# Kernel optimization log

Measured on AMD Instinct MI355X. Metric: run time of the kernel, lower is better.

The kernel has to match this reference:

```python
import jax, jax.numpy as jnp
import numpy as np

T, B, D, H = 512, 64, 512, 512

def setup_inputs() -> dict:
    key = jax.random.key(0)
    ks = jax.random.split(key, 14)
    s = 0.02
    inp = {
        "inputs": jax.random.normal(ks[0], (T, B, D), dtype=jnp.float32),
        # gate linears: weight [D+H, H] (transposed torch layout), bias [H]
        "Wf": jax.random.normal(ks[1], (D + H, H), dtype=jnp.float32) * s,
        "bf": jax.random.normal(ks[2], (H,), dtype=jnp.float32) * s,
        "Wi": jax.random.normal(ks[3], (D + H, H), dtype=jnp.float32) * s,
        "bi": jax.random.normal(ks[4], (H,), dtype=jnp.float32) * s,
        "Wg": jax.random.normal(ks[5], (D + H, H), dtype=jnp.float32) * s,
        "bg": jax.random.normal(ks[6], (H,), dtype=jnp.float32) * s,
        "Wo": jax.random.normal(ks[7], (D + H, H), dtype=jnp.float32) * s,
        "bo": jax.random.normal(ks[8], (H,), dtype=jnp.float32) * s,
        # residual linears on hidden state: [H, H], no bias
        "Rf": jax.random.normal(ks[9], (H, H), dtype=jnp.float32) * s,
        "Ri": jax.random.normal(ks[10], (H, H), dtype=jnp.float32) * s,
        "Rg": jax.random.normal(ks[11], (H, H), dtype=jnp.float32) * s,
        "Ro": jax.random.normal(ks[12], (H, H), dtype=jnp.float32) * s,
    }
    return inp


def reference(inputs, Wf, bf, Wi, bi, Wg, bg, Wo, bo, Rf, Ri, Rg, Ro):
    # QLSTM forward (eval mode, gate_dropout inactive). states=None -> zeros.
    batch = inputs.shape[1]
    hidden = Wf.shape[1]
    h0 = jnp.zeros((batch, hidden), dtype=inputs.dtype)
    c0 = jnp.zeros((batch, hidden), dtype=inputs.dtype)

    # Fuse the 4 gate GEMMs into one [D+H, 4H] matmul and the 4 residual
    # GEMMs into one [H, 4H] matmul (same math, fewer launches).
    W4 = jnp.concatenate([Wf, Wi, Wg, Wo], axis=1)   # [D+H, 4H]
    b4 = jnp.concatenate([bf, bi, bg, bo], axis=0)   # [4H]
    R4 = jnp.concatenate([Rf, Ri, Rg, Ro], axis=1)   # [H, 4H]

    def step(carry, x):
        hx, cx = carry
        combined = jnp.concatenate([x, hx], axis=1)            # [B, D+H]
        z = combined @ W4 + b4 + hx @ R4                        # [B, 4H]
        f, i, g, o = jnp.split(z, 4, axis=1)
        f = jax.nn.sigmoid(f)
        i = jax.nn.sigmoid(i)
        g = jnp.tanh(g)
        o = jax.nn.sigmoid(o)
        cx = f * cx + i * g
        hx = o * jnp.tanh(cx)
        return (hx, cx), hx

    (hx, cx), stacked = jax.lax.scan(step, (h0, c0), inputs)
    return stacked, hx, cx
```

## Files before the change

kernel.cpp:

```cpp
#include <hip/hip_runtime.h>
#include <hip/hip_bf16.h>

typedef __attribute__((ext_vector_type(8))) short s16x8;
typedef __attribute__((ext_vector_type(4))) float f32x4;

__device__ __forceinline__ ushort f2bf(float x) {
  __hip_bfloat16 b = __float2bfloat16(x);
  return *reinterpret_cast<ushort*>(&b);
}

__device__ __forceinline__ float sigm_fast(float z) {
  return __builtin_amdgcn_rcpf(1.0f + __builtin_amdgcn_exp2f(z * -1.44269504088896f));
}

__global__ __launch_bounds__(256) void pack_weights(
    const float* __restrict__ Wf, const float* __restrict__ Wi,
    const float* __restrict__ Wg, const float* __restrict__ Wo,
    const float* __restrict__ Rf, const float* __restrict__ Ri,
    const float* __restrict__ Rg, const float* __restrict__ Ro,
    const float* __restrict__ bfp, const float* __restrict__ bip,
    const float* __restrict__ bgp, const float* __restrict__ bop,
    ushort* __restrict__ Wx, ushort* __restrict__ Rs, float* __restrict__ bp)
{
  const int p = blockIdx.x * 8 + (threadIdx.x >> 5);
  const int kk = (threadIdx.x & 31) * 16;
  const int gate = p & 3;
  const int hcol = (p >> 5) * 8 + ((p >> 4) & 1) * 4 + ((p & 15) >> 2);
  const float* W = (gate == 0) ? Wf : (gate == 1) ? Wi : (gate == 2) ? Wg : Wo;
  const float* R = (gate == 0) ? Rf : (gate == 1) ? Ri : (gate == 2) ? Rg : Ro;
  union { ushort u[16]; s16x8 v[2]; } wb, rb;
#pragma unroll
  for (int e = 0; e < 16; ++e) {
    const int k = kk + e;
    wb.u[e] = f2bf(W[(size_t)k * 512 + hcol]);
    rb.u[e] = f2bf(W[(size_t)(512 + k) * 512 + hcol] + R[(size_t)k * 512 + hcol]);
  }
  *(s16x8*)(Wx + (size_t)p * 512 + kk)     = wb.v[0];
  *(s16x8*)(Wx + (size_t)p * 512 + kk + 8) = wb.v[1];
  *(s16x8*)(Rs + (size_t)p * 512 + kk)     = rb.v[0];
  *(s16x8*)(Rs + (size_t)p * 512 + kk + 8) = rb.v[1];
  if ((threadIdx.x & 31) == 0) {
    const float* B = (gate == 0) ? bfp : (gate == 1) ? bip : (gate == 2) ? bgp : bop;
    bp[p] = B[hcol];
  }
}

__global__ __launch_bounds__(256) void swizzle_x(
    const float* __restrict__ x, ushort* __restrict__ xsw)
{
  __shared__ ushort xl[64 * 520];
  const int t = blockIdx.x;
  const int tid = threadIdx.x;
  const float4* x4 = (const float4*)(x + (size_t)t * 32768);
#pragma unroll 4
  for (int j = 0; j < 32; ++j) {
    const int i4 = j * 256 + tid;
    const float4 v = x4[i4];
    const int base = i4 * 4;
    const int row = base >> 9;
    const int col = base & 511;
    ushort4 u;
    u.x = f2bf(v.x); u.y = f2bf(v.y); u.z = f2bf(v.z); u.w = f2bf(v.w);
    *(ushort4*)(&xl[row * 520 + col]) = u;
  }
  __syncthreads();
#pragma unroll 4
  for (int j = 0; j < 16; ++j) {
    const int F = j * 256 + tid;
    const int l = F & 63;
    const int kc = (F >> 6) & 15;
    const int mt = F >> 10;
    const int row = mt * 16 + (l & 15);
    const int k0 = kc * 32 + (l >> 4) * 8;
    const s16x8 v = *(const s16x8*)(&xl[row * 520 + k0]);
    *(s16x8*)(&xsw[((size_t)t * 4096 + F) * 8]) = v;
  }
}

__global__ __launch_bounds__(512, 1) void zx_gemm(
    const ushort* __restrict__ xsw, const ushort* __restrict__ Wx,
    float* __restrict__ zx, int t0, int tcnt)
{
  __shared__ ushort lbuf[32768];
  const int pg = blockIdx.x;
  const int tgrp = blockIdx.y;
  const int tid = threadIdx.x;
  const int wid = tid >> 6;
  const int lane = tid & 63;
  const int mpair = wid >> 2;
  const int np = wid & 3;
  const int q = pg * 4 + np;
  const int l15 = lane & 15;
  const int hi = lane >> 4;

  s16x8 Bg[2][16];
#pragma unroll
  for (int nt = 0; nt < 2; ++nt)
#pragma unroll
    for (int kc = 0; kc < 16; ++kc)
      Bg[nt][kc] = *(const s16x8*)(Wx + (size_t)(q * 32 + nt * 16 + l15) * 512 + kc * 32 + hi * 8);

  for (int tt = 0; tt < tcnt; ++tt) {
    const int tl = tgrp * tcnt + tt;
    const int t = t0 + tl;
#pragma unroll
    for (int j = 0; j < 8; ++j) {
      const int fid = j * 512 + tid;
      *(s16x8*)(&lbuf[(size_t)fid * 8]) =
          *(const s16x8*)(xsw + ((size_t)t * 4096 + fid) * 8);
    }
    __syncthreads();
#pragma unroll
    for (int a = 0; a < 2; ++a) {
      const int mt = mpair * 2 + a;
      f32x4 acc0 = {0.f, 0.f, 0.f, 0.f};
      f32x4 acc1 = {0.f, 0.f, 0.f, 0.f};
#pragma unroll
      for (int kc = 0; kc < 16; ++kc) {
        const s16x8 af = *(const s16x8*)(&lbuf[((size_t)(mt * 16 + kc) * 64 + lane) * 8]);
        acc0 = __builtin_amdgcn_mfma_f32_16x16x32_bf16(af, Bg[0][kc], acc0, 0, 0, 0);
        acc1 = __builtin_amdgcn_mfma_f32_16x16x32_bf16(af, Bg[1][kc], acc1, 0, 0, 0);
      }
      float* o = zx + ((((size_t)tl * 4 + mt) * 64 + q) * 64 + lane) * 8;
      *(f32x4*)(o)     = acc0;
      *(f32x4*)(o + 4) = acc1;
    }
    __syncthreads();
  }
}

__global__ __launch_bounds__(512, 1) void rec_kernel(
    const ushort* __restrict__ Rs, const float* __restrict__ bp,
    const float* __restrict__ zx, ushort* __restrict__ hbuf,
    float* __restrict__ csave, int* __restrict__ cnt,
    float* __restrict__ dout, int t0, int CH)
{
  __shared__ ushort hsl[8192];
  const int bid = blockIdx.x;
  const int g = bid & 3;
  const int tid = threadIdx.x;
  const int wid = tid >> 6;
  const int lane = tid & 63;
  const int q = (bid >> 2) * 8 + wid;
  const int gate = lane & 3;
  const int l15 = lane & 15;
  const int hi = lane >> 4;

  s16x8 Brg[2][16];
#pragma unroll
  for (int nt = 0; nt < 2; ++nt)
#pragma unroll
    for (int kc = 0; kc < 16; ++kc)
      Brg[nt][kc] = *(const s16x8*)(Rs + (size_t)(q * 32 + nt * 16 + l15) * 512 + kc * 32 + hi * 8);

  const float b0 = bp[q * 32 + l15];
  const float b1 = bp[q * 32 + 16 + l15];

  float cst[2][4];
  float* csp = csave + ((size_t)(bid * 8 + wid) * 64 + lane) * 8;
  if (t0 == 0) {
#pragma unroll
    for (int i = 0; i < 2; ++i)
#pragma unroll
      for (int r = 0; r < 4; ++r) cst[i][r] = 0.0f;
  } else {
#pragma unroll
    for (int i = 0; i < 2; ++i)
#pragma unroll
      for (int r = 0; r < 4; ++r) cst[i][r] = csp[i * 4 + r];
  }

  const int srow = hi * 4 + gate;
  const int hcol0 = q * 8 + (l15 >> 2);

  const int crow = tid >> 5;
  const int cbyte = (tid & 31) * 32;
  const int cswz = (crow & 7) << 4;
  const int abase = l15 * 1024 + hi * 16;
  const int aswz = (l15 & 7) << 4;

  int* const cptr = cnt + g * 64;

  const float* zp = zx + ((((size_t)0 * 4 + g) * 64 + q) * 64 + lane) * 8;
  float4 z0 = *(const float4*)zp;
  float4 z1 = *(const float4*)(zp + 4);

  for (int tl = 0; tl < CH; ++tl) {
    const int t = t0 + tl;

    if (tl > 0) {
      const int target = t * 8;
      while (__hip_atomic_load(cptr, __ATOMIC_RELAXED, __HIP_MEMORY_SCOPE_AGENT) < target) {}
      asm volatile("" ::: "memory");
    }

    {
      const ushort* hsrc = hbuf + ((size_t)tl * 4 + g) * 8192;
      const s16x8 v0 = *(const s16x8*)(hsrc + crow * 512 + (cbyte >> 1));
      const s16x8 v1 = *(const s16x8*)(hsrc + crow * 512 + (cbyte >> 1) + 8);
      *(s16x8*)(&hsl[(crow * 1024 + (cbyte ^ cswz)) >> 1]) = v0;
      *(s16x8*)(&hsl[(crow * 1024 + ((cbyte + 16) ^ cswz)) >> 1]) = v1;
    }
    __syncthreads();

    f32x4 acc0 = {0.f, 0.f, 0.f, 0.f};
    f32x4 acc1 = {0.f, 0.f, 0.f, 0.f};
#pragma unroll
    for (int kc = 0; kc < 16; ++kc) {
      const s16x8 a = *(const s16x8*)(&hsl[((abase + kc * 64) ^ aswz) >> 1]);
      acc0 = __builtin_amdgcn_mfma_f32_16x16x32_bf16(a, Brg[0][kc], acc0, 0, 0, 0);
      acc1 = __builtin_amdgcn_mfma_f32_16x16x32_bf16(a, Brg[1][kc], acc1, 0, 0, 0);
    }

    float h_out[2][4];
#pragma unroll
    for (int nt = 0; nt < 2; ++nt) {
#pragma unroll
      for (int r = 0; r < 4; ++r) {
        float z = (nt ? acc1[r] : acc0[r]);
        z += nt ? ((r == 0) ? z1.x : (r == 1) ? z1.y : (r == 2) ? z1.z : z1.w)
                : ((r == 0) ? z0.x : (r == 1) ? z0.y : (r == 2) ? z0.z : z0.w);
        z += nt ? b1 : b0;
        const float zz = (gate == 2) ? z + z : z;
        const float s = sigm_fast(zz);
        const float act = (gate == 2) ? (s + s - 1.0f) : s;
        const int ai = __float_as_int(act);
        const float fv = __int_as_float(__builtin_amdgcn_mov_dpp(ai, 0x00, 0xF, 0xF, true));
        const float iv = __int_as_float(__builtin_amdgcn_mov_dpp(ai, 0x55, 0xF, 0xF, true));
        const float gv = __int_as_float(__builtin_amdgcn_mov_dpp(ai, 0xAA, 0xF, 0xF, true));
        const float ov = __int_as_float(__builtin_amdgcn_mov_dpp(ai, 0xFF, 0xF, 0xF, true));
        const float cn = fmaf(fv, cst[nt][r], iv * gv);
        cst[nt][r] = cn;
        const float s2 = sigm_fast(cn + cn);
        h_out[nt][r] = ov * (s2 + s2 - 1.0f);
      }
    }

    float hv[2], cv[2];
#pragma unroll
    for (int nt = 0; nt < 2; ++nt) {
      hv[nt] = (gate == 0) ? h_out[nt][0] : (gate == 1) ? h_out[nt][1]
             : (gate == 2) ? h_out[nt][2] : h_out[nt][3];
      cv[nt] = (gate == 0) ? cst[nt][0] : (gate == 1) ? cst[nt][1]
             : (gate == 2) ? cst[nt][2] : cst[nt][3];
    }

    {
      ushort* hn = hbuf + ((size_t)(tl + 1) * 4 + g) * 8192;
#pragma unroll
      for (int nt = 0; nt < 2; ++nt)
        __hip_atomic_store(&hn[srow * 512 + hcol0 + nt * 4], f2bf(hv[nt]),
                           __ATOMIC_RELAXED, __HIP_MEMORY_SCOPE_AGENT);
      if (tl == CH - 1) {
        ushort* h0 = hbuf + (size_t)g * 8192;
#pragma unroll
        for (int nt = 0; nt < 2; ++nt)
          h0[srow * 512 + hcol0 + nt * 4] = f2bf(hv[nt]);
      }
    }
    asm volatile("s_waitcnt vmcnt(0)" ::: "memory");
    __syncthreads();
    if (tid == 0)
      __hip_atomic_fetch_add(cptr, 1, __ATOMIC_RELAXED, __HIP_MEMORY_SCOPE_AGENT);

    if (tl + 1 < CH) {
      const float* zn = zx + ((((size_t)(tl + 1) * 4 + g) * 64 + q) * 64 + lane) * 8;
      z0 = *(const float4*)zn;
      z1 = *(const float4*)(zn + 4);
    }
    {
      const size_t drow = (size_t)(g * 16 + srow) * 512;
#pragma unroll
      for (int nt = 0; nt < 2; ++nt)
        dout[(size_t)t * 32768 + drow + hcol0 + nt * 4] = hv[nt];
      if (t == 511) {
#pragma unroll
        for (int nt = 0; nt < 2; ++nt) {
          dout[(size_t)16777216 + drow + hcol0 + nt * 4] = hv[nt];
          dout[(size_t)16809984 + drow + hcol0 + nt * 4] = cv[nt];
        }
      }
    }
  }

#pragma unroll
  for (int i = 0; i < 2; ++i)
#pragma unroll
    for (int r = 0; r < 4; ++r) csp[i * 4 + r] = cst[i][r];
}

extern "C" void kernel_launch(void* const* d_in, const int* in_sizes, int n_in,
                              void* d_out, int out_size, void* d_ws, size_t ws_size,
                              hipStream_t stream)
{
  const float* x   = (const float*)d_in[0];
  const float* Wf  = (const float*)d_in[1];
  const float* bfp = (const float*)d_in[2];
  const float* Wi  = (const float*)d_in[3];
  const float* bip = (const float*)d_in[4];
  const float* Wg  = (const float*)d_in[5];
  const float* bgp = (const float*)d_in[6];
  const float* Wo  = (const float*)d_in[7];
  const float* bop = (const float*)d_in[8];
  const float* Rf  = (const float*)d_in[9];
  const float* Ri  = (const float*)d_in[10];
  const float* Rg  = (const float*)d_in[11];
  const float* Ro  = (const float*)d_in[12];
  float* dout = (float*)d_out;
  char* ws = (char*)d_ws;

  const size_t o_Wx  = 0;
  const size_t o_Rs  = o_Wx + 2097152;
  const size_t o_bp  = o_Rs + 2097152;
  const size_t o_xsw = o_bp + 8192;
  const size_t o_zx  = o_xsw + 33554432;

  int CH = 64;
  while (CH > 4) {
    const size_t need = o_zx + (size_t)CH * 524288 + (size_t)(CH + 1) * 65536
                      + 524288 + 1024;
    if (need <= ws_size) break;
    CH >>= 1;
  }
  const size_t o_hb = o_zx + (size_t)CH * 524288;
  const size_t o_cs = o_hb + (size_t)(CH + 1) * 65536;
  const size_t o_fl = o_cs + 524288;

  ushort* Wx  = (ushort*)(ws + o_Wx);
  ushort* Rs  = (ushort*)(ws + o_Rs);
  float*  bp  = (float*)(ws + o_bp);
  ushort* xsw = (ushort*)(ws + o_xsw);
  float*  zx  = (float*)(ws + o_zx);
  ushort* hb  = (ushort*)(ws + o_hb);
  float*  csv = (float*)(ws + o_cs);
  int*    fl  = (int*)(ws + o_fl);

  pack_weights<<<256, 256, 0, stream>>>(Wf, Wi, Wg, Wo, Rf, Ri, Rg, Ro,
                                        bfp, bip, bgp, bop, Wx, Rs, bp);
  swizzle_x<<<512, 256, 0, stream>>>(x, xsw);
  hipMemsetAsync(hb, 0, 65536, stream);
  hipMemsetAsync(fl, 0, 1024, stream);

  const int nch = 512 / CH;
  for (int c = 0; c < nch; ++c) {
    const int G = (CH < 16) ? CH : 16;
    zx_gemm<<<dim3(16, G), 512, 0, stream>>>(xsw, Wx, zx, c * CH, CH / G);
    rec_kernel<<<32, 512, 0, stream>>>(Rs, bp, zx, hb, csv, fl, dout, c * CH, CH);
  }
}
```

Measured before the change: 1.787 ms.

## Process two batch groups per block with interleaved recurrent steps on half the blocks

The recurrent kernel now launches 16 blocks instead of 32. Each block handles two batch groups (A and B) and interleaves their recurrent GEMM, gate math and publish phases, so the wait on one group's flag overlaps with compute for the other. Hidden-state publishing is staged through shared memory and written as 64-bit atomic stores from 16 lanes instead of scattered 16-bit stores, and the counter stride changes. The risk is that per-step serial work per block doubles, which can lengthen the critical path. The layout of the saved c-state also changes.

New measurement: 3.144 ms. 76.0% more time.

```diff
diff --git a/kernel.cpp b/kernel.cpp
--- a/kernel.cpp
+++ b/kernel.cpp
@@ -135,39 +135,47 @@
     float* __restrict__ csave, int* __restrict__ cnt,
     float* __restrict__ dout, int t0, int CH)
 {
-  __shared__ ushort hsl[8192];
+  __shared__ ushort hslA[8192];
+  __shared__ ushort hslB[8192];
+  __shared__ ushort tbuf[1024];
+
   const int bid = blockIdx.x;
-  const int g = bid & 3;
+  const int team = bid >> 3;
   const int tid = threadIdx.x;
   const int wid = tid >> 6;
   const int lane = tid & 63;
-  const int q = (bid >> 2) * 8 + wid;
+  const int q = (bid & 7) * 8 + wid;
+  const int gA = team * 2;
+  const int gB = team * 2 + 1;
   const int gate = lane & 3;
   const int l15 = lane & 15;
   const int hi = lane >> 4;
 
-  s16x8 Brg[2][16];
+  f32x4 Brg[2][16];
 #pragma unroll
   for (int nt = 0; nt < 2; ++nt)
 #pragma unroll
-    for (int kc = 0; kc < 16; ++kc)
-      Brg[nt][kc] = *(const s16x8*)(Rs + (size_t)(q * 32 + nt * 16 + l15) * 512 + kc * 32 + hi * 8);
+    for (int kc = 0; kc < 16; ++kc) {
+      Brg[nt][kc] = *(const f32x4*)(Rs + (size_t)(q * 32 + nt * 16 + l15) * 512 + kc * 32 + hi * 8);
+      asm volatile("" : "+v"(Brg[nt][kc]));
+    }
 
   const float b0 = bp[q * 32 + l15];
   const float b1 = bp[q * 32 + 16 + l15];
 
-  float cst[2][4];
-  float* csp = csave + ((size_t)(bid * 8 + wid) * 64 + lane) * 8;
+  float cA[2][4], cB[2][4];
+  float* cspA = csave + ((size_t)((bid * 8 + wid) * 64 + lane) * 2 + 0) * 8;
+  float* cspB = cspA + 8;
   if (t0 == 0) {
 #pragma unroll
     for (int i = 0; i < 2; ++i)
 #pragma unroll
-      for (int r = 0; r < 4; ++r) cst[i][r] = 0.0f;
+      for (int r = 0; r < 4; ++r) { cA[i][r] = 0.0f; cB[i][r] = 0.0f; }
   } else {
 #pragma unroll
     for (int i = 0; i < 2; ++i)
 #pragma unroll
-      for (int r = 0; r < 4; ++r) cst[i][r] = csp[i * 4 + r];
+      for (int r = 0; r < 4; ++r) { cA[i][r] = cspA[i * 4 + r]; cB[i][r] = cspB[i * 4 + r]; }
   }
 
   const int srow = hi * 4 + gate;
@@ -176,117 +184,174 @@
   const int crow = tid >> 5;
   const int cbyte = (tid & 31) * 32;
   const int cswz = (crow & 7) << 4;
+  const int srcofs = crow * 512 + (cbyte >> 1);
+  const int wofs0 = (crow * 1024 + (cbyte ^ cswz)) >> 1;
+  const int wofs1 = (crow * 1024 + ((cbyte + 16) ^ cswz)) >> 1;
   const int abase = l15 * 1024 + hi * 16;
   const int aswz = (l15 & 7) << 4;
 
-  int* const cptr = cnt + g * 64;
-
-  const float* zp = zx + ((((size_t)0 * 4 + g) * 64 + q) * 64 + lane) * 8;
-  float4 z0 = *(const float4*)zp;
-  float4 z1 = *(const float4*)(zp + 4);
+  int* const cptrA = cnt + gA * 16;
+  int* const cptrB = cnt + gB * 16;
+
+  const float* zpA = zx + (((size_t)0 * 4 + gA) * 64 + q) * 64 * 8 + (size_t)lane * 8;
+  const float* zpB = zx + (((size_t)0 * 4 + gB) * 64 + q) * 64 * 8 + (size_t)lane * 8;
+  float4 zA0 = *(const float4*)zpA, zA1 = *(const float4*)(zpA + 4);
+  float4 zB0 = *(const float4*)zpB, zB1 = *(const float4*)(zpB + 4);
+
+#define GATES(ACC0, ACC1, Z0, Z1, CST, HV0, HV1, CV0, CV1)                      \
+  {                                                                              \
+    float h_[2][4];                                                              \
+    _Pragma("unroll")                                                            \
+    for (int nt = 0; nt < 2; ++nt) {                                             \
+      _Pragma("unroll")                                                          \
+      for (int r = 0; r < 4; ++r) {                                              \
+        float z = (nt ? (ACC1)[r] : (ACC0)[r]);                                  \
+        z += nt ? ((r==0)?(Z1).x:(r==1)?(Z1).y:(r==2)?(Z1).z:(Z1).w)             \
+                : ((r==0)?(Z0).x:(r==1)?(Z0).y:(r==2)?(Z0).z:(Z0).w);            \
+        z += nt ? b1 : b0;                                                       \
+        const float zz = (gate == 2) ? z + z : z;                                \
+        const float s = sigm_fast(zz);                                           \
+        const float act = (gate == 2) ? (s + s - 1.0f) : s;                      \
+        const int ai = __float_as_int(act);                                      \
+        const float fv = __int_as_float(__builtin_amdgcn_mov_dpp(ai, 0x00, 0xF, 0xF, true)); \
+        const float iv = __int_as_float(__builtin_amdgcn_mov_dpp(ai, 0x55, 0xF, 0xF, true)); \
+        const float gv = __int_as_float(__builtin_amdgcn_mov_dpp(ai, 0xAA, 0xF, 0xF, true)); \
+        const float ov = __int_as_float(__builtin_amdgcn_mov_dpp(ai, 0xFF, 0xF, 0xF, true)); \
+        const float cn = fmaf(fv, CST[nt][r], iv * gv);                          \
+        CST[nt][r] = cn;                                                         \
+        const float s2 = sigm_fast(cn + cn);                                     \
+        h_[nt][r] = ov * (s2 + s2 - 1.0f);                                       \
+      }                                                                          \
+    }                                                                            \
+    HV0 = (gate==0)?h_[0][0]:(gate==1)?h_[0][1]:(gate==2)?h_[0][2]:h_[0][3];     \
+    HV1 = (gate==0)?h_[1][0]:(gate==1)?h_[1][1]:(gate==2)?h_[1][2]:h_[1][3];     \
+    CV0 = (gate==0)?CST[0][0]:(gate==1)?CST[0][1]:(gate==2)?CST[0][2]:CST[0][3]; \
+    CV1 = (gate==0)?CST[1][0]:(gate==1)?CST[1][1]:(gate==2)?CST[1][2]:CST[1][3]; \
+  }
+
+#define PUBLISH(HV0, HV1, SLOT, CPTR)                                            \
+  {                                                                              \
+    tbuf[wid * 128 + srow * 8 + (l15 >> 2)]     = f2bf(HV0);                     \
+    tbuf[wid * 128 + srow * 8 + (l15 >> 2) + 4] = f2bf(HV1);                     \
+    asm volatile("s_waitcnt lgkmcnt(0)" ::: "memory");                           \
+    __builtin_amdgcn_sched_barrier(0);                                           \
+    if (lane < 16) {                                                             \
+      const unsigned long long* rp = (const unsigned long long*)&tbuf[wid * 128 + lane * 8]; \
+      ushort* dst = (SLOT) + lane * 512 + q * 8;                                 \
+      __hip_atomic_store((unsigned long long*)dst, rp[0],                        \
+                         __ATOMIC_RELAXED, __HIP_MEMORY_SCOPE_AGENT);            \
+      __hip_atomic_store((unsigned long long*)(dst + 4), rp[1],                  \
+                         __ATOMIC_RELAXED, __HIP_MEMORY_SCOPE_AGENT);            \
+    }                                                                            \
+    asm volatile("s_waitcnt vmcnt(0)" ::: "memory");                             \
+    __syncthreads();                                                             \
+    if (tid == 0)                                                                \
+      __hip_atomic_fetch_add((CPTR), 1, __ATOMIC_RELAXED, __HIP_MEMORY_SCOPE_AGENT); \
+  }
 
   for (int tl = 0; tl < CH; ++tl) {
     const int t = t0 + tl;
 
     if (tl > 0) {
-      const int target = t * 8;
-      while (__hip_atomic_load(cptr, __ATOMIC_RELAXED, __HIP_MEMORY_SCOPE_AGENT) < target) {}
+      const int tgt = 8 * t;
+      while (__hip_atomic_load(cptrA, __ATOMIC_RELAXED, __HIP_MEMORY_SCOPE_AGENT) < tgt) {}
       asm volatile("" ::: "memory");
     }
-
+    const ushort* hsA = hbuf + ((size_t)tl * 4 + gA) * 8192;
+    const s16x8 la0 = *(const s16x8*)(hsA + srcofs);
+    const s16x8 la1 = *(const s16x8*)(hsA + srcofs + 8);
+    if (tl > 0) {
+      const int tgt = 8 * t;
+      while (__hip_atomic_load(cptrB, __ATOMIC_RELAXED, __HIP_MEMORY_SCOPE_AGENT) < tgt) {}
+      asm volatile("" ::: "memory");
+    }
+    const ushort* hsB = hbuf + ((size_t)tl * 4 + gB) * 8192;
+    const s16x8 lb0 = *(const s16x8*)(hsB + srcofs);
+    const s16x8 lb1 = *(const s16x8*)(hsB + srcofs + 8);
+
+    *(s16x8*)(&hslA[wofs0]) = la0;
+    *(s16x8*)(&hslA[wofs1]) = la1;
+    __syncthreads();
+    f32x4 ac0 = {0.f, 0.f, 0.f, 0.f};
+    f32x4 ac1 = {0.f, 0.f, 0.f, 0.f};
+#pragma unroll
+    for (int kc = 0; kc < 16; ++kc) {
+      const s16x8 a = *(const s16x8*)(&hslA[((abase + kc * 64) ^ aswz) >> 1]);
+      ac0 = __builtin_amdgcn_mfma_f32_16x16x32_bf16(a, __builtin_bit_cast(s16x8, Brg[0][kc]), ac0, 0, 0, 0);
+      ac1 = __builtin_amdgcn_mfma_f32_16x16x32_bf16(a, __builtin_bit_cast(s16x8, Brg[1][kc]), ac1, 0, 0, 0);
+    }
+    float hvA0, hvA1, cvA0, cvA1;
+    GATES(ac0, ac1, zA0, zA1, cA, hvA0, hvA1, cvA0, cvA1);
     {
-      const ushort* hsrc = hbuf + ((size_t)tl * 4 + g) * 8192;
-      const s16x8 v0 = *(const s16x8*)(hsrc + crow * 512 + (cbyte >> 1));
-      const s16x8 v1 = *(const s16x8*)(hsrc + crow * 512 + (cbyte >> 1) + 8);
-      *(s16x8*)(&hsl[(crow * 1024 + (cbyte ^ cswz)) >> 1]) = v0;
-      *(s16x8*)(&hsl[(crow * 1024 + ((cbyte + 16) ^ cswz)) >> 1]) = v1;
-    }
+      ushort* hn = hbuf + ((size_t)(tl + 1) * 4 + gA) * 8192;
+      PUBLISH(hvA0, hvA1, hn, cptrA);
+    }
+    {
+      const size_t drow = (size_t)(gA * 16 + srow) * 512;
+      dout[(size_t)t * 32768 + drow + hcol0]     = hvA0;
+      dout[(size_t)t * 32768 + drow + hcol0 + 4] = hvA1;
+      if (t == 511) {
+        dout[(size_t)16777216 + drow + hcol0]     = hvA0;
+        dout[(size_t)16777216 + drow + hcol0 + 4] = hvA1;
+        dout[(size_t)16809984 + drow + hcol0]     = cvA0;
+        dout[(size_t)16809984 + drow + hcol0 + 4] = cvA1;
+      }
+      if (tl == CH - 1) {
+        ushort* h0 = hbuf + (size_t)gA * 8192;
+        h0[srow * 512 + hcol0]     = f2bf(hvA0);
+        h0[srow * 512 + hcol0 + 4] = f2bf(hvA1);
+      } else {
+        const float* zn = zx + ((((size_t)(tl + 1) * 4 + gA) * 64 + q) * 64 + lane) * 8;
+        zA0 = *(const float4*)zn;
+        zA1 = *(const float4*)(zn + 4);
+      }
+    }
+
+    *(s16x8*)(&hslB[wofs0]) = lb0;
+    *(s16x8*)(&hslB[wofs1]) = lb1;
     __syncthreads();
-
-    f32x4 acc0 = {0.f, 0.f, 0.f, 0.f};
-    f32x4 acc1 = {0.f, 0.f, 0.f, 0.f};
+    f32x4 bc0 = {0.f, 0.f, 0.f, 0.f};
+    f32x4 bc1 = {0.f, 0.f, 0.f, 0.f};
 #pragma unroll
     for (int kc = 0; kc < 16; ++kc) {
-      const s16x8 a = *(const s16x8*)(&hsl[((abase + kc * 64) ^ aswz) >> 1]);
-      acc0 = __builtin_amdgcn_mfma_f32_16x16x32_bf16(a, Brg[0][kc], acc0, 0, 0, 0);
-      acc1 = __builtin_amdgcn_mfma_f32_16x16x32_bf16(a, Brg[1][kc], acc1, 0, 0, 0);
-    }
-
-    float h_out[2][4];
-#pragma unroll
-    for (int nt = 0; nt < 2; ++nt) {
-#pragma unroll
-      for (int r = 0; r < 4; ++r) {
-        float z = (nt ? acc1[r] : acc0[r]);
-        z += nt ? ((r == 0) ? z1.x : (r == 1) ? z1.y : (r == 2) ? z1.z : z1.w)
-                : ((r == 0) ? z0.x : (r == 1) ? z0.y : (r == 2) ? z0.z : z0.w);
-        z += nt ? b1 : b0;
-        const float zz = (gate == 2) ? z + z : z;
-        const float s = sigm_fast(zz);
-        const float act = (gate == 2) ? (s + s - 1.0f) : s;
-        const int ai = __float_as_int(act);
-        const float fv = __int_as_float(__builtin_amdgcn_mov_dpp(ai, 0x00, 0xF, 0xF, true));
-        const float iv = __int_as_float(__builtin_amdgcn_mov_dpp(ai, 0x55, 0xF, 0xF, true));
-        const float gv = __int_as_float(__builtin_amdgcn_mov_dpp(ai, 0xAA, 0xF, 0xF, true));
-        const float ov = __int_as_float(__builtin_amdgcn_mov_dpp(ai, 0xFF, 0xF, 0xF, true));
-        const float cn = fmaf(fv, cst[nt][r], iv * gv);
-        cst[nt][r] = cn;
-        const float s2 = sigm_fast(cn + cn);
-        h_out[nt][r] = ov * (s2 + s2 - 1.0f);
+      const s16x8 a = *(const s16x8*)(&hslB[((abase + kc * 64) ^ aswz) >> 1]);
+      bc0 = __builtin_amdgcn_mfma_f32_16x16x32_bf16(a, __builtin_bit_cast(s16x8, Brg[0][kc]), bc0, 0, 0, 0);
+      bc1 = __builtin_amdgcn_mfma_f32_16x16x32_bf16(a, __builtin_bit_cast(s16x8, Brg[1][kc]), bc1, 0, 0, 0);
+    }
+    float hvB0, hvB1, cvB0, cvB1;
+    GATES(bc0, bc1, zB0, zB1, cB, hvB0, hvB1, cvB0, cvB1);
+    {
+      ushort* hn = hbuf + ((size_t)(tl + 1) * 4 + gB) * 8192;
+      PUBLISH(hvB0, hvB1, hn, cptrB);
+    }
+    {
+      const size_t drow = (size_t)(gB * 16 + srow) * 512;
+      dout[(size_t)t * 32768 + drow + hcol0]     = hvB0;
+      dout[(size_t)t * 32768 + drow + hcol0 + 4] = hvB1;
+      if (t == 511) {
+        dout[(size_t)16777216 + drow + hcol0]     = hvB0;
+        dout[(size_t)16777216 + drow + hcol0 + 4] = hvB1;
+        dout[(size_t)16809984 + drow + hcol0]     = cvB0;
+        dout[(size_t)16809984 + drow + hcol0 + 4] = cvB1;
       }
-    }
-
-    float hv[2], cv[2];
-#pragma unroll
-    for (int nt = 0; nt < 2; ++nt) {
-      hv[nt] = (gate == 0) ? h_out[nt][0] : (gate == 1) ? h_out[nt][1]
-             : (gate == 2) ? h_out[nt][2] : h_out[nt][3];
-      cv[nt] = (gate == 0) ? cst[nt][0] : (gate == 1) ? cst[nt][1]
-             : (gate == 2) ? cst[nt][2] : cst[nt][3];
-    }
-
-    {
-      ushort* hn = hbuf + ((size_t)(tl + 1) * 4 + g) * 8192;
-#pragma unroll
-      for (int nt = 0; nt < 2; ++nt)
-        __hip_atomic_store(&hn[srow * 512 + hcol0 + nt * 4], f2bf(hv[nt]),
-                           __ATOMIC_RELAXED, __HIP_MEMORY_SCOPE_AGENT);
       if (tl == CH - 1) {
-        ushort* h0 = hbuf + (size_t)g * 8192;
-#pragma unroll
-        for (int nt = 0; nt < 2; ++nt)
-          h0[srow * 512 + hcol0 + nt * 4] = f2bf(hv[nt]);
+        ushort* h0 = hbuf + (size_t)gB * 8192;
+        h0[srow * 512 + hcol0]     = f2bf(hvB0);
+        h0[srow * 512 + hcol0 + 4] = f2bf(hvB1);
+      } else {
+        const float* zn = zx + ((((size_t)(tl + 1) * 4 + gB) * 64 + q) * 64 + lane) * 8;
+        zB0 = *(const float4*)zn;
+        zB1 = *(const float4*)(zn + 4);
       }
     }
-    asm volatile("s_waitcnt vmcnt(0)" ::: "memory");
-    __syncthreads();
-    if (tid == 0)
-      __hip_atomic_fetch_add(cptr, 1, __ATOMIC_RELAXED, __HIP_MEMORY_SCOPE_AGENT);
-
-    if (tl + 1 < CH) {
-      const float* zn = zx + ((((size_t)(tl + 1) * 4 + g) * 64 + q) * 64 + lane) * 8;
-      z0 = *(const float4*)zn;
-      z1 = *(const float4*)(zn + 4);
-    }
-    {
-      const size_t drow = (size_t)(g * 16 + srow) * 512;
-#pragma unroll
-      for (int nt = 0; nt < 2; ++nt)
-        dout[(size_t)t * 32768 + drow + hcol0 + nt * 4] = hv[nt];
-      if (t == 511) {
-#pragma unroll
-        for (int nt = 0; nt < 2; ++nt) {
-          dout[(size_t)16777216 + drow + hcol0 + nt * 4] = hv[nt];
-          dout[(size_t)16809984 + drow + hcol0 + nt * 4] = cv[nt];
-        }
-      }
-    }
   }
 
 #pragma unroll
   for (int i = 0; i < 2; ++i)
 #pragma unroll
-    for (int r = 0; r < 4; ++r) csp[i * 4 + r] = cst[i][r];
+    for (int r = 0; r < 4; ++r) { cspA[i * 4 + r] = cA[i][r]; cspB[i * 4 + r] = cB[i][r]; }
+#undef GATES
+#undef PUBLISH
 }
 
 extern "C" void kernel_launch(void* const* d_in, const int* in_sizes, int n_in,
@@ -345,6 +410,6 @@
   for (int c = 0; c < nch; ++c) {
     const int G = (CH < 16) ? CH : 16;
     zx_gemm<<<dim3(16, G), 512, 0, stream>>>(xsw, Wx, zx, c * CH, CH / G);
-    rec_kernel<<<32, 512, 0, stream>>>(Rs, bp, zx, hb, csv, fl, dout, c * CH, CH);
-  }
-}
+    rec_kernel<<<16, 512, 0, stream>>>(Rs, bp, zx, hb, csv, fl, dout, c * CH, CH);
+  }
+}
```

## Fuse input GEMM with recurrence and overlap next chunk's projection

Applied to the files above, without the earlier changes.

Merges the x-swizzle, input-projection GEMM and recurrent kernel into one launch. 32 blocks run the recurrence for the current chunk while 128 other blocks compute the next chunk's input projection into a double-buffered bf16 zx buffer. The recurrence also changes in several ways. The shared atomic counter becomes per-block flags polled with a wave-wide all, groups are regrouped by batch, and h is packed through LDS into 64-bit stores. The strided fp32 output writes are moved to a separate reorder kernel that reads a bf16 h log. In exchange it adds a priming launch, bf16 rounding of zx and the output, and extra workspace.

After: 1.722 ms. 3.6% less time.

```diff
diff --git a/kernel.cpp b/kernel.cpp
--- a/kernel.cpp
+++ b/kernel.cpp
@@ -8,7 +8,9 @@
   __hip_bfloat16 b = __float2bfloat16(x);
   return *reinterpret_cast<ushort*>(&b);
 }
-
+__device__ __forceinline__ float bf2f(ushort u) {
+  union { unsigned int i; float f; } c; c.i = ((unsigned int)u) << 16; return c.f;
+}
 __device__ __forceinline__ float sigm_fast(float z) {
   return __builtin_amdgcn_rcpf(1.0f + __builtin_amdgcn_exp2f(z * -1.44269504088896f));
 }
@@ -45,114 +47,89 @@
   }
 }
 
-__global__ __launch_bounds__(256) void swizzle_x(
-    const float* __restrict__ x, ushort* __restrict__ xsw)
+__global__ __launch_bounds__(512, 1) void fused_kernel(
+    const float* __restrict__ x, const ushort* __restrict__ Wx,
+    const ushort* __restrict__ Rs, const float* __restrict__ bp,
+    const ushort* __restrict__ zxr, ushort* __restrict__ zxw,
+    ushort* __restrict__ hbuf, float* __restrict__ csave,
+    int* __restrict__ flags, ushort* __restrict__ hsave,
+    float* __restrict__ cfinal, int t0, int CH, int zxt0, int do_rec)
 {
-  __shared__ ushort xl[64 * 520];
-  const int t = blockIdx.x;
-  const int tid = threadIdx.x;
-  const float4* x4 = (const float4*)(x + (size_t)t * 32768);
-#pragma unroll 4
-  for (int j = 0; j < 32; ++j) {
-    const int i4 = j * 256 + tid;
-    const float4 v = x4[i4];
-    const int base = i4 * 4;
-    const int row = base >> 9;
-    const int col = base & 511;
-    ushort4 u;
-    u.x = f2bf(v.x); u.y = f2bf(v.y); u.z = f2bf(v.z); u.w = f2bf(v.w);
-    *(ushort4*)(&xl[row * 520 + col]) = u;
-  }
-  __syncthreads();
-#pragma unroll 4
-  for (int j = 0; j < 16; ++j) {
-    const int F = j * 256 + tid;
-    const int l = F & 63;
-    const int kc = (F >> 6) & 15;
-    const int mt = F >> 10;
-    const int row = mt * 16 + (l & 15);
-    const int k0 = kc * 32 + (l >> 4) * 8;
-    const s16x8 v = *(const s16x8*)(&xl[row * 520 + k0]);
-    *(s16x8*)(&xsw[((size_t)t * 4096 + F) * 8]) = v;
-  }
-}
-
-__global__ __launch_bounds__(512, 1) void zx_gemm(
-    const ushort* __restrict__ xsw, const ushort* __restrict__ Wx,
-    float* __restrict__ zx, int t0, int tcnt)
-{
-  __shared__ ushort lbuf[32768];
-  const int pg = blockIdx.x;
-  const int tgrp = blockIdx.y;
+  __shared__ ushort lds_u[33280];
   const int tid = threadIdx.x;
   const int wid = tid >> 6;
   const int lane = tid & 63;
-  const int mpair = wid >> 2;
-  const int np = wid & 3;
-  const int q = pg * 4 + np;
   const int l15 = lane & 15;
   const int hi = lane >> 4;
 
-  s16x8 Bg[2][16];
+  if (blockIdx.x >= 32) {
+    if (zxt0 >= 512) return;
+    const int zbid = blockIdx.x - 32;
+    const int pg = zbid & 15;
+    const int ts = zbid >> 4;
+    const int mpair = wid >> 2;
+    const int np = wid & 3;
+    const int q = pg * 4 + np;
+    s16x8 Bg[2][16];
+#pragma unroll
+    for (int nt = 0; nt < 2; ++nt)
+#pragma unroll
+      for (int kc = 0; kc < 16; ++kc)
+        Bg[nt][kc] = *(const s16x8*)(Wx + (size_t)(q * 32 + nt * 16 + l15) * 512 + kc * 32 + hi * 8);
+    const int tper = CH >> 3;
+    for (int tt = 0; tt < tper; ++tt) {
+      const int tl = ts * tper + tt;
+      const int t = zxt0 + tl;
+      const float4* x4 = (const float4*)(x + (size_t)t * 32768);
+#pragma unroll
+      for (int j = 0; j < 16; ++j) {
+        const int i4 = j * 512 + tid;
+        const float4 v = x4[i4];
+        const int row = i4 >> 7;
+        const int c0 = (i4 & 127) * 4;
+        ushort4 u;
+        u.x = f2bf(v.x); u.y = f2bf(v.y); u.z = f2bf(v.z); u.w = f2bf(v.w);
+        *(ushort4*)(&lds_u[row * 520 + c0]) = u;
+      }
+      __syncthreads();
+#pragma unroll
+      for (int a = 0; a < 2; ++a) {
+        const int mt = mpair * 2 + a;
+        f32x4 a0 = {0.f, 0.f, 0.f, 0.f};
+        f32x4 a1 = {0.f, 0.f, 0.f, 0.f};
+#pragma unroll
+        for (int kc = 0; kc < 16; ++kc) {
+          const s16x8 af = *(const s16x8*)(&lds_u[(mt * 16 + l15) * 520 + kc * 32 + hi * 8]);
+          a0 = __builtin_amdgcn_mfma_f32_16x16x32_bf16(af, Bg[0][kc], a0, 0, 0, 0);
+          a1 = __builtin_amdgcn_mfma_f32_16x16x32_bf16(af, Bg[1][kc], a1, 0, 0, 0);
+        }
+        union { ushort u[8]; s16x8 v; } ub;
+#pragma unroll
+        for (int r = 0; r < 4; ++r) { ub.u[r] = f2bf(a0[r]); ub.u[4 + r] = f2bf(a1[r]); }
+        *(s16x8*)(zxw + ((((size_t)tl * 4 + mt) * 64 + q) * 64 + lane) * 8) = ub.v;
+      }
+      __syncthreads();
+    }
+    return;
+  }
+
+  if (!do_rec) return;
+  ushort* hsl = lds_u;
+  ushort* tbuf = lds_u + 8192;
+  const int bid = blockIdx.x;
+  const int g = bid >> 3;
+  const int mem = bid & 7;
+  const int q = mem * 8 + wid;
+  const int gate = lane & 3;
+
+  f32x4 Brg[2][16];
 #pragma unroll
   for (int nt = 0; nt < 2; ++nt)
 #pragma unroll
-    for (int kc = 0; kc < 16; ++kc)
-      Bg[nt][kc] = *(const s16x8*)(Wx + (size_t)(q * 32 + nt * 16 + l15) * 512 + kc * 32 + hi * 8);
-
-  for (int tt = 0; tt < tcnt; ++tt) {
-    const int tl = tgrp * tcnt + tt;
-    const int t = t0 + tl;
-#pragma unroll
-    for (int j = 0; j < 8; ++j) {
-      const int fid = j * 512 + tid;
-      *(s16x8*)(&lbuf[(size_t)fid * 8]) =
-          *(const s16x8*)(xsw + ((size_t)t * 4096 + fid) * 8);
-    }
-    __syncthreads();
-#pragma unroll
-    for (int a = 0; a < 2; ++a) {
-      const int mt = mpair * 2 + a;
-      f32x4 acc0 = {0.f, 0.f, 0.f, 0.f};
-      f32x4 acc1 = {0.f, 0.f, 0.f, 0.f};
-#pragma unroll
-      for (int kc = 0; kc < 16; ++kc) {
-        const s16x8 af = *(const s16x8*)(&lbuf[((size_t)(mt * 16 + kc) * 64 + lane) * 8]);
-        acc0 = __builtin_amdgcn_mfma_f32_16x16x32_bf16(af, Bg[0][kc], acc0, 0, 0, 0);
-        acc1 = __builtin_amdgcn_mfma_f32_16x16x32_bf16(af, Bg[1][kc], acc1, 0, 0, 0);
-      }
-      float* o = zx + ((((size_t)tl * 4 + mt) * 64 + q) * 64 + lane) * 8;
-      *(f32x4*)(o)     = acc0;
-      *(f32x4*)(o + 4) = acc1;
-    }
-    __syncthreads();
-  }
-}
-
-__global__ __launch_bounds__(512, 1) void rec_kernel(
-    const ushort* __restrict__ Rs, const float* __restrict__ bp,
-    const float* __restrict__ zx, ushort* __restrict__ hbuf,
-    float* __restrict__ csave, int* __restrict__ cnt,
-    float* __restrict__ dout, int t0, int CH)
-{
-  __shared__ ushort hsl[8192];
-  const int bid = blockIdx.x;
-  const int g = bid & 3;
-  const int tid = threadIdx.x;
-  const int wid = tid >> 6;
-  const int lane = tid & 63;
-  const int q = (bid >> 2) * 8 + wid;
-  const int gate = lane & 3;
-  const int l15 = lane & 15;
-  const int hi = lane >> 4;
-
-  s16x8 Brg[2][16];
-#pragma unroll
-  for (int nt = 0; nt < 2; ++nt)
-#pragma unroll
-    for (int kc = 0; kc < 16; ++kc)
-      Brg[nt][kc] = *(const s16x8*)(Rs + (size_t)(q * 32 + nt * 16 + l15) * 512 + kc * 32 + hi * 8);
-
+    for (int kc = 0; kc < 16; ++kc) {
+      Brg[nt][kc] = *(const f32x4*)(Rs + (size_t)(q * 32 + nt * 16 + l15) * 512 + kc * 32 + hi * 8);
+      asm volatile("" : "+v"(Brg[nt][kc]));
+    }
   const float b0 = bp[q * 32 + l15];
   const float b1 = bp[q * 32 + 16 + l15];
 
@@ -172,55 +149,54 @@
 
   const int srow = hi * 4 + gate;
   const int hcol0 = q * 8 + (l15 >> 2);
-
   const int crow = tid >> 5;
   const int cbyte = (tid & 31) * 32;
   const int cswz = (crow & 7) << 4;
+  const int srcofs = crow * 512 + (cbyte >> 1);
+  const int wofs0 = (crow * 1024 + (cbyte ^ cswz)) >> 1;
+  const int wofs1 = (crow * 1024 + ((cbyte + 16) ^ cswz)) >> 1;
   const int abase = l15 * 1024 + hi * 16;
   const int aswz = (l15 & 7) << 4;
-
-  int* const cptr = cnt + g * 64;
-
-  const float* zp = zx + ((((size_t)0 * 4 + g) * 64 + q) * 64 + lane) * 8;
-  float4 z0 = *(const float4*)zp;
-  float4 z1 = *(const float4*)(zp + 4);
+  int* const myflag = &flags[(g * 8 + mem) * 16];
+  const int pollofs = (g * 8 + (lane & 7)) * 16;
 
   for (int tl = 0; tl < CH; ++tl) {
     const int t = t0 + tl;
-
     if (tl > 0) {
-      const int target = t * 8;
-      while (__hip_atomic_load(cptr, __ATOMIC_RELAXED, __HIP_MEMORY_SCOPE_AGENT) < target) {}
+      asm volatile("s_waitcnt vmcnt(0)" ::: "memory");
+      __syncthreads();
+      if (tid == 0)
+        __hip_atomic_store(myflag, t, __ATOMIC_RELAXED, __HIP_MEMORY_SCOPE_AGENT);
+    }
+    const s16x8 zv = *(const s16x8*)(zxr + ((((size_t)tl * 4 + g) * 64 + q) * 64 + lane) * 8);
+    if (tl > 0) {
+      int v;
+      do {
+        v = __hip_atomic_load(&flags[pollofs], __ATOMIC_RELAXED, __HIP_MEMORY_SCOPE_AGENT);
+      } while (!__all(v >= t));
       asm volatile("" ::: "memory");
     }
-
-    {
-      const ushort* hsrc = hbuf + ((size_t)tl * 4 + g) * 8192;
-      const s16x8 v0 = *(const s16x8*)(hsrc + crow * 512 + (cbyte >> 1));
-      const s16x8 v1 = *(const s16x8*)(hsrc + crow * 512 + (cbyte >> 1) + 8);
-      *(s16x8*)(&hsl[(crow * 1024 + (cbyte ^ cswz)) >> 1]) = v0;
-      *(s16x8*)(&hsl[(crow * 1024 + ((cbyte + 16) ^ cswz)) >> 1]) = v1;
-    }
+    const ushort* hs = hbuf + ((size_t)tl * 4 + g) * 8192;
+    const s16x8 h0 = *(const s16x8*)(hs + srcofs);
+    const s16x8 h1 = *(const s16x8*)(hs + srcofs + 8);
+    *(s16x8*)(&hsl[wofs0]) = h0;
+    *(s16x8*)(&hsl[wofs1]) = h1;
     __syncthreads();
-
-    f32x4 acc0 = {0.f, 0.f, 0.f, 0.f};
-    f32x4 acc1 = {0.f, 0.f, 0.f, 0.f};
+    f32x4 a0 = {0.f, 0.f, 0.f, 0.f};
+    f32x4 a1 = {0.f, 0.f, 0.f, 0.f};
 #pragma unroll
     for (int kc = 0; kc < 16; ++kc) {
-      const s16x8 a = *(const s16x8*)(&hsl[((abase + kc * 64) ^ aswz) >> 1]);
-      acc0 = __builtin_amdgcn_mfma_f32_16x16x32_bf16(a, Brg[0][kc], acc0, 0, 0, 0);
-      acc1 = __builtin_amdgcn_mfma_f32_16x16x32_bf16(a, Brg[1][kc], acc1, 0, 0, 0);
-    }
-
-    float h_out[2][4];
+      const s16x8 af = *(const s16x8*)(&hsl[((abase + kc * 64) ^ aswz) >> 1]);
+      a0 = __builtin_amdgcn_mfma_f32_16x16x32_bf16(af, __builtin_bit_cast(s16x8, Brg[0][kc]), a0, 0, 0, 0);
+      a1 = __builtin_amdgcn_mfma_f32_16x16x32_bf16(af, __builtin_bit_cast(s16x8, Brg[1][kc]), a1, 0, 0, 0);
+    }
+    float hv[2], cv[2];
 #pragma unroll
     for (int nt = 0; nt < 2; ++nt) {
+      float hr[4];
 #pragma unroll
       for (int r = 0; r < 4; ++r) {
-        float z = (nt ? acc1[r] : acc0[r]);
-        z += nt ? ((r == 0) ? z1.x : (r == 1) ? z1.y : (r == 2) ? z1.z : z1.w)
-                : ((r == 0) ? z0.x : (r == 1) ? z0.y : (r == 2) ? z0.z : z0.w);
-        z += nt ? b1 : b0;
+        float z = (nt ? a1[r] : a0[r]) + bf2f((ushort)zv[nt * 4 + r]) + (nt ? b1 : b0);
         const float zz = (gate == 2) ? z + z : z;
         const float s = sigm_fast(zz);
         const float act = (gate == 2) ? (s + s - 1.0f) : s;
@@ -232,61 +208,96 @@
         const float cn = fmaf(fv, cst[nt][r], iv * gv);
         cst[nt][r] = cn;
         const float s2 = sigm_fast(cn + cn);
-        h_out[nt][r] = ov * (s2 + s2 - 1.0f);
+        hr[r] = ov * (s2 + s2 - 1.0f);
       }
-    }
-
-    float hv[2], cv[2];
-#pragma unroll
-    for (int nt = 0; nt < 2; ++nt) {
-      hv[nt] = (gate == 0) ? h_out[nt][0] : (gate == 1) ? h_out[nt][1]
-             : (gate == 2) ? h_out[nt][2] : h_out[nt][3];
+      hv[nt] = (gate == 0) ? hr[0] : (gate == 1) ? hr[1] : (gate == 2) ? hr[2] : hr[3];
       cv[nt] = (gate == 0) ? cst[nt][0] : (gate == 1) ? cst[nt][1]
              : (gate == 2) ? cst[nt][2] : cst[nt][3];
     }
-
-    {
-      ushort* hn = hbuf + ((size_t)(tl + 1) * 4 + g) * 8192;
-#pragma unroll
-      for (int nt = 0; nt < 2; ++nt)
-        __hip_atomic_store(&hn[srow * 512 + hcol0 + nt * 4], f2bf(hv[nt]),
+    const ushort pb0 = f2bf(hv[0]), pb1 = f2bf(hv[1]);
+    tbuf[wid * 128 + srow * 8 + (l15 >> 2)]     = pb0;
+    tbuf[wid * 128 + srow * 8 + (l15 >> 2) + 4] = pb1;
+    asm volatile("s_waitcnt lgkmcnt(0)" ::: "memory");
+    __builtin_amdgcn_sched_barrier(0);
+    if (tl != CH - 1) {
+      if (lane < 16) {
+        const unsigned long long* rp = (const unsigned long long*)&tbuf[wid * 128 + lane * 8];
+        ushort* dst = hbuf + ((size_t)(tl + 1) * 4 + g) * 8192 + lane * 512 + q * 8;
+        __hip_atomic_store((unsigned long long*)dst, rp[0],
                            __ATOMIC_RELAXED, __HIP_MEMORY_SCOPE_AGENT);
-      if (tl == CH - 1) {
-        ushort* h0 = hbuf + (size_t)g * 8192;
-#pragma unroll
-        for (int nt = 0; nt < 2; ++nt)
-          h0[srow * 512 + hcol0 + nt * 4] = f2bf(hv[nt]);
+        __hip_atomic_store((unsigned long long*)(dst + 4), rp[1],
+                           __ATOMIC_RELAXED, __HIP_MEMORY_SCOPE_AGENT);
       }
-    }
-    asm volatile("s_waitcnt vmcnt(0)" ::: "memory");
-    __syncthreads();
-    if (tid == 0)
-      __hip_atomic_fetch_add(cptr, 1, __ATOMIC_RELAXED, __HIP_MEMORY_SCOPE_AGENT);
-
-    if (tl + 1 < CH) {
-      const float* zn = zx + ((((size_t)(tl + 1) * 4 + g) * 64 + q) * 64 + lane) * 8;
-      z0 = *(const float4*)zn;
-      z1 = *(const float4*)(zn + 4);
-    }
-    {
-      const size_t drow = (size_t)(g * 16 + srow) * 512;
-#pragma unroll
-      for (int nt = 0; nt < 2; ++nt)
-        dout[(size_t)t * 32768 + drow + hcol0 + nt * 4] = hv[nt];
-      if (t == 511) {
-#pragma unroll
-        for (int nt = 0; nt < 2; ++nt) {
-          dout[(size_t)16777216 + drow + hcol0 + nt * 4] = hv[nt];
-          dout[(size_t)16809984 + drow + hcol0 + nt * 4] = cv[nt];
-        }
-      }
-    }
-  }
-
+    } else {
+      ushort* hn0 = hbuf + (size_t)g * 8192;
+      hn0[srow * 512 + hcol0]     = pb0;
+      hn0[srow * 512 + hcol0 + 4] = pb1;
+    }
+    ushort2 hp; hp.x = pb0; hp.y = pb1;
+    *(ushort2*)(hsave + (((size_t)t * 4 + g) * 8 + mem) * 1024 + wid * 128 + lane * 2) = hp;
+    if (t == 511) {
+      float* cf = cfinal + (((size_t)(g * 8 + mem) * 8 + wid) * 64 + lane) * 2;
+      cf[0] = cv[0]; cf[1] = cv[1];
+    }
+  }
 #pragma unroll
   for (int i = 0; i < 2; ++i)
 #pragma unroll
     for (int r = 0; r < 4; ++r) csp[i * 4 + r] = cst[i][r];
+}
+
+__global__ __launch_bounds__(256) void reorder_kernel(
+    const ushort* __restrict__ hsave, const float* __restrict__ cfinal,
+    float* __restrict__ dout)
+{
+  __shared__ ushort lds[8192];
+  const int t = blockIdx.x;
+  const int g = blockIdx.y;
+  const int tid = threadIdx.x;
+  const s16x8* src = (const s16x8*)(hsave + ((size_t)t * 4 + g) * 8192);
+#pragma unroll
+  for (int j = 0; j < 4; ++j) {
+    const int i = j * 256 + tid;
+    *(s16x8*)(&lds[i * 8]) = src[i];
+  }
+  __syncthreads();
+  const int srow = tid >> 4;
+  const int cb = (tid & 15) * 32;
+  float buf[32];
+#pragma unroll
+  for (int cc = 0; cc < 32; ++cc) {
+    const int col = cb + cc;
+    const int q = col >> 3;
+    const int memb = q >> 3;
+    const int wd = q & 7;
+    const int nt = (col >> 2) & 1;
+    const int l15v = ((col & 3) << 2) | (srow & 3);
+    const int lanev = ((srow >> 2) << 4) | l15v;
+    buf[cc] = bf2f(lds[memb * 1024 + wd * 128 + lanev * 2 + nt]);
+  }
+  float* o = dout + (size_t)t * 32768 + (size_t)(g * 16 + srow) * 512 + cb;
+#pragma unroll
+  for (int j = 0; j < 8; ++j) *(float4*)(o + j * 4) = *(const float4*)(&buf[j * 4]);
+  if (t == 511) {
+    float* oh = dout + (size_t)16777216 + (size_t)(g * 16 + srow) * 512 + cb;
+#pragma unroll
+    for (int j = 0; j < 8; ++j) *(float4*)(oh + j * 4) = *(const float4*)(&buf[j * 4]);
+    float cbuf[32];
+#pragma unroll
+    for (int cc = 0; cc < 32; ++cc) {
+      const int col = cb + cc;
+      const int q = col >> 3;
+      const int memb = q >> 3;
+      const int wd = q & 7;
+      const int nt = (col >> 2) & 1;
+      const int l15v = ((col & 3) << 2) | (srow & 3);
+      const int lanev = ((srow >> 2) << 4) | l15v;
+      cbuf[cc] = cfinal[(((size_t)(g * 8 + memb) * 8 + wd) * 64 + lanev) * 2 + nt];
+    }
+    float* oc = dout + (size_t)16809984 + (size_t)(g * 16 + srow) * 512 + cb;
+#pragma unroll
+    for (int j = 0; j < 8; ++j) *(float4*)(oc + j * 4) = *(const float4*)(&cbuf[j * 4]);
+  }
 }
 
 extern "C" void kernel_launch(void* const* d_in, const int* in_sizes, int n_in,
@@ -309,42 +320,50 @@
   float* dout = (float*)d_out;
   char* ws = (char*)d_ws;
 
-  const size_t o_Wx  = 0;
-  const size_t o_Rs  = o_Wx + 2097152;
-  const size_t o_bp  = o_Rs + 2097152;
-  const size_t o_xsw = o_bp + 8192;
-  const size_t o_zx  = o_xsw + 33554432;
+  const size_t o_Wx = 0;
+  const size_t o_Rs = 2097152;
+  const size_t o_bp = 4194304;
+  const size_t o_z0 = o_bp + 8192;
 
   int CH = 64;
-  while (CH > 4) {
-    const size_t need = o_zx + (size_t)CH * 524288 + (size_t)(CH + 1) * 65536
-                      + 524288 + 1024;
-    if (need <= ws_size) break;
+  for (;;) {
+    const size_t need = o_z0 + 2 * (size_t)CH * 262144 + (size_t)(CH + 1) * 65536
+                      + 524288 + 2048 + 33554432 + 131072;
+    if (need <= ws_size || CH <= 8) break;
     CH >>= 1;
   }
-  const size_t o_hb = o_zx + (size_t)CH * 524288;
+  const size_t zsz  = (size_t)CH * 262144;
+  const size_t o_z1 = o_z0 + zsz;
+  const size_t o_hb = o_z1 + zsz;
   const size_t o_cs = o_hb + (size_t)(CH + 1) * 65536;
   const size_t o_fl = o_cs + 524288;
-
-  ushort* Wx  = (ushort*)(ws + o_Wx);
-  ushort* Rs  = (ushort*)(ws + o_Rs);
-  float*  bp  = (float*)(ws + o_bp);
-  ushort* xsw = (ushort*)(ws + o_xsw);
-  float*  zx  = (float*)(ws + o_zx);
-  ushort* hb  = (ushort*)(ws + o_hb);
-  float*  csv = (float*)(ws + o_cs);
-  int*    fl  = (int*)(ws + o_fl);
+  const size_t o_hs = o_fl + 2048;
+  const size_t o_cf = o_hs + 33554432;
+
+  ushort* Wx   = (ushort*)(ws + o_Wx);
+  ushort* Rs   = (ushort*)(ws + o_Rs);
+  float*  bp   = (float*)(ws + o_bp);
+  ushort* zx0  = (ushort*)(ws + o_z0);
+  ushort* zx1  = (ushort*)(ws + o_z1);
+  ushort* hb   = (ushort*)(ws + o_hb);
+  float*  csv  = (float*)(ws + o_cs);
+  int*    fl   = (int*)(ws + o_fl);
+  ushort* hsv  = (ushort*)(ws + o_hs);
+  float*  cfin = (float*)(ws + o_cf);
 
   pack_weights<<<256, 256, 0, stream>>>(Wf, Wi, Wg, Wo, Rf, Ri, Rg, Ro,
                                         bfp, bip, bgp, bop, Wx, Rs, bp);
-  swizzle_x<<<512, 256, 0, stream>>>(x, xsw);
   hipMemsetAsync(hb, 0, 65536, stream);
-  hipMemsetAsync(fl, 0, 1024, stream);
-
+  hipMemsetAsync(fl, 0, 2048, stream);
+
+  fused_kernel<<<160, 512, 0, stream>>>(x, Wx, Rs, bp, zx1, zx0, hb, csv, fl,
+                                        hsv, cfin, 0, CH, 0, 0);
   const int nch = 512 / CH;
   for (int c = 0; c < nch; ++c) {
-    const int G = (CH < 16) ? CH : 16;
-    zx_gemm<<<dim3(16, G), 512, 0, stream>>>(xsw, Wx, zx, c * CH, CH / G);
-    rec_kernel<<<32, 512, 0, stream>>>(Rs, bp, zx, hb, csv, fl, dout, c * CH, CH);
-  }
-}
+    const ushort* zr = (c & 1) ? zx1 : zx0;
+    ushort* zw       = (c & 1) ? zx0 : zx1;
+    fused_kernel<<<160, 512, 0, stream>>>(x, Wx, Rs, bp, zr, zw, hb, csv, fl,
+                                          hsv, cfin, c * CH, CH, (c + 1) * CH, 1);
+  }
+  reorder_kernel<<<dim3(512, 4), 256, 0, stream>>>(hsv, cfin, dout);
+}
```
